# Kernel tuning notes

Hardware: AMD Instinct MI355X
Metric: run time of the kernel (lower is better)

Reference implementation:

```python
import jax, jax.numpy as jnp
import numpy as np

N = 50000
D_IN = 512
D_OUT = 512
NUM_SAMPLE = 2


def setup_inputs() -> dict:
    key = jax.random.key(0)
    ks = jax.random.split(key, 8)
    x = jax.random.normal(ks[0], (N, D_IN), dtype=jnp.float32)
    neighs1 = jax.random.randint(ks[1], (N, NUM_SAMPLE), 0, N, dtype=jnp.int32)
    neighs2 = jax.random.randint(ks[2], (N, NUM_SAMPLE), 0, N, dtype=jnp.int32)
    # SageLayer weights: [out, 2*in] (self || aggregated neighbors), xavier-ish scale
    W1 = jax.random.normal(ks[3], (D_OUT, 2 * D_IN), dtype=jnp.float32) * 0.03
    W2 = jax.random.normal(ks[4], (D_OUT, 2 * D_OUT), dtype=jnp.float32) * 0.03
    fc_w = jax.random.normal(ks[5], (2, N * D_OUT), dtype=jnp.float32) * 0.0005
    fc_b = jnp.zeros((2,), dtype=jnp.float32)
    return {"x": x, "neighs1": neighs1, "neighs2": neighs2,
            "W1": W1, "W2": W2, "fc_w": fc_w, "fc_b": fc_b}


def _sage_layer(h, neighs, W):
    # MEAN aggregation over the num_sample sampled neighbors (self excluded, gcn=False).
    # Equivalent to the original dense one-hot mask.div(num_neigh).mm(embed_matrix).
    agg = h[neighs].mean(axis=1)                      # [N, S, d] -> [N, d]
    combined = jnp.concatenate([h, agg], axis=1)      # [N, 2d]
    # F.relu(W.mm(combined.t())).t() == relu(combined @ W.T)
    return jax.nn.relu(combined @ W.T)                # [N, out]


def reference(x, neighs1, neighs2, W1, W2, fc_w, fc_b):
    h = _sage_layer(x, neighs1, W1)
    h = _sage_layer(h, neighs2, W2)
    flat = h.reshape(1, -1)                           # [1, N*out]
    logits = flat @ fc_w.T + fc_b                     # [1, 2]
    return (flat, jax.nn.log_softmax(logits, axis=1))
```

## Files before the change

### kernel.cpp

```cpp
#include <hip/hip_runtime.h>
#include <stdint.h>

typedef short bf16x8 __attribute__((ext_vector_type(8)));
typedef float f32x4 __attribute__((ext_vector_type(4)));
typedef unsigned short u16x8 __attribute__((ext_vector_type(8)));

#define N_NODES 50000
#define DIM 512
#define KDIM 1024
#define NPAD 50048
#define M_TILES 391
#define N_TILES 4
#define FLAT_TOTAL 25600000ULL

__device__ __forceinline__ unsigned short f2bf(float f) {
    unsigned u = __float_as_uint(f);
    unsigned r = u + 0x7FFFu + ((u >> 16) & 1u);
    return (unsigned short)(r >> 16);
}
__device__ __forceinline__ float bf2f(unsigned short h) {
    return __uint_as_float(((unsigned)h) << 16);
}

__device__ __forceinline__ void llds16(const void* g, void* l) {
    __builtin_amdgcn_global_load_lds(
        (const __attribute__((address_space(1))) void*)g,
        (__attribute__((address_space(3))) void*)l,
        16, 0, 0);
}

__global__ void cast_w(const float* __restrict__ w, unsigned short* __restrict__ o) {
    int i = (blockIdx.x * blockDim.x + threadIdx.x) * 8;
    float4 v0 = *(const float4*)&w[i];
    float4 v1 = *(const float4*)&w[i + 4];
    u16x8 r;
    r[0] = f2bf(v0.x); r[1] = f2bf(v0.y); r[2] = f2bf(v0.z); r[3] = f2bf(v0.w);
    r[4] = f2bf(v1.x); r[5] = f2bf(v1.y); r[6] = f2bf(v1.z); r[7] = f2bf(v1.w);
    *(u16x8*)&o[i] = r;
}

__global__ void build_a1(const float* __restrict__ x, const int* __restrict__ nb,
                         unsigned short* __restrict__ A) {
    int i = blockIdx.x;
    int t = threadIdx.x;
    u16x8 o;
    if (t < 64) {
        int c = t * 8;
        const float4* p = (const float4*)&x[(size_t)i * DIM + c];
        float4 a = p[0], b = p[1];
        o[0] = f2bf(a.x); o[1] = f2bf(a.y); o[2] = f2bf(a.z); o[3] = f2bf(a.w);
        o[4] = f2bf(b.x); o[5] = f2bf(b.y); o[6] = f2bf(b.z); o[7] = f2bf(b.w);
        *(u16x8*)&A[(size_t)i * KDIM + c] = o;
    } else {
        int c = (t - 64) * 8;
        int n0 = nb[i * 2], n1 = nb[i * 2 + 1];
        const float4* p0 = (const float4*)&x[(size_t)n0 * DIM + c];
        const float4* p1 = (const float4*)&x[(size_t)n1 * DIM + c];
        float4 a0 = p0[0], a1 = p0[1], b0 = p1[0], b1 = p1[1];
        o[0] = f2bf((a0.x + b0.x) * 0.5f); o[1] = f2bf((a0.y + b0.y) * 0.5f);
        o[2] = f2bf((a0.z + b0.z) * 0.5f); o[3] = f2bf((a0.w + b0.w) * 0.5f);
        o[4] = f2bf((a1.x + b1.x) * 0.5f); o[5] = f2bf((a1.y + b1.y) * 0.5f);
        o[6] = f2bf((a1.z + b1.z) * 0.5f); o[7] = f2bf((a1.w + b1.w) * 0.5f);
        *(u16x8*)&A[(size_t)i * KDIM + DIM + c] = o;
    }
}

__global__ void build_a2(const unsigned short* __restrict__ h, const int* __restrict__ nb,
                         unsigned short* __restrict__ A) {
    int i = blockIdx.x;
    int t = threadIdx.x;
    if (t < 64) {
        int c = t * 8;
        *(u16x8*)&A[(size_t)i * KDIM + c] = *(const u16x8*)&h[(size_t)i * DIM + c];
    } else {
        int c = (t - 64) * 8;
        int n0 = nb[i * 2], n1 = nb[i * 2 + 1];
        u16x8 a = *(const u16x8*)&h[(size_t)n0 * DIM + c];
        u16x8 b = *(const u16x8*)&h[(size_t)n1 * DIM + c];
        u16x8 o;
#pragma unroll
        for (int j = 0; j < 8; j++) o[j] = f2bf((bf2f(a[j]) + bf2f(b[j])) * 0.5f);
        *(u16x8*)&A[(size_t)i * KDIM + DIM + c] = o;
    }
}

template <int OUT_MODE>
__global__ __launch_bounds__(256)
void gemm_bt(const unsigned short* __restrict__ A, const unsigned short* __restrict__ B,
             void* __restrict__ C) {
    __shared__ unsigned short As[128 * 32];
    __shared__ unsigned short Bs[128 * 32];

    int t = threadIdx.x;
    int bm = blockIdx.x >> 2;
    int bn = blockIdx.x & 3;
    int lane = t & 63;
    int wave = t >> 6;
    int m_off = (wave >> 1) * 64;
    int n_off = (wave & 1) * 64;
    int lrow = lane & 15;
    int lk = (lane >> 4) * 8;

    f32x4 acc[4][4];
#pragma unroll
    for (int i = 0; i < 4; i++)
#pragma unroll
        for (int j = 0; j < 4; j++) acc[i][j] = (f32x4){0.f, 0.f, 0.f, 0.f};

    const unsigned short* ga = A + (size_t)(bm * 128 + (t >> 2)) * KDIM + (t & 3) * 8;
    const unsigned short* gb = B + (size_t)(bn * 128 + (t >> 2)) * KDIM + (t & 3) * 8;

    for (int k0 = 0; k0 < KDIM; k0 += 32) {
        __syncthreads();
        llds16(ga + k0, &As[t * 8]);
        llds16(ga + k0 + 64 * KDIM, &As[t * 8 + 2048]);
        llds16(gb + k0, &Bs[t * 8]);
        llds16(gb + k0 + 64 * KDIM, &Bs[t * 8 + 2048]);
        __syncthreads();

        bf16x8 af[4], bfr[4];
#pragma unroll
        for (int i = 0; i < 4; i++)
            af[i] = *(const bf16x8*)&As[(m_off + i * 16 + lrow) * 32 + lk];
#pragma unroll
        for (int j = 0; j < 4; j++)
            bfr[j] = *(const bf16x8*)&Bs[(n_off + j * 16 + lrow) * 32 + lk];
#pragma unroll
        for (int i = 0; i < 4; i++)
#pragma unroll
            for (int j = 0; j < 4; j++)
                acc[i][j] = __builtin_amdgcn_mfma_f32_16x16x32_bf16(af[i], bfr[j], acc[i][j], 0, 0, 0);
    }

    int lc = lane & 15;
    int lr = (lane >> 4) << 2;
#pragma unroll
    for (int i = 0; i < 4; i++) {
        int row0 = bm * 128 + m_off + i * 16 + lr;
#pragma unroll
        for (int j = 0; j < 4; j++) {
            int col = bn * 128 + n_off + j * 16 + lc;
            f32x4 v = acc[i][j];
            if (OUT_MODE == 0) {
                unsigned short* Cb = (unsigned short*)C;
#pragma unroll
                for (int r = 0; r < 4; r++)
                    Cb[(size_t)(row0 + r) * DIM + col] = f2bf(fmaxf(v[r], 0.f));
            } else {
                float* Cf = (float*)C;
#pragma unroll
                for (int r = 0; r < 4; r++)
                    if (row0 + r < N_NODES)
                        Cf[(size_t)(row0 + r) * DIM + col] = fmaxf(v[r], 0.f);
            }
        }
    }
}

__global__ void zero2(float* p) { if (threadIdx.x < 2) p[threadIdx.x] = 0.f; }

__global__ void fc_reduce(const float* __restrict__ flat, const float* __restrict__ fcw,
                          float* __restrict__ partials) {
    float s0 = 0.f, s1 = 0.f;
    size_t stride = (size_t)gridDim.x * blockDim.x * 4;
    for (size_t i = ((size_t)blockIdx.x * blockDim.x + threadIdx.x) * 4; i < FLAT_TOTAL; i += stride) {
        float4 v  = *(const float4*)&flat[i];
        float4 w0 = *(const float4*)&fcw[i];
        float4 w1 = *(const float4*)&fcw[FLAT_TOTAL + i];
        s0 += v.x * w0.x + v.y * w0.y + v.z * w0.z + v.w * w0.w;
        s1 += v.x * w1.x + v.y * w1.y + v.z * w1.z + v.w * w1.w;
    }
#pragma unroll
    for (int off = 32; off > 0; off >>= 1) {
        s0 += __shfl_down(s0, off);
        s1 += __shfl_down(s1, off);
    }
    __shared__ float r0[4], r1[4];
    int lane = threadIdx.x & 63, w = threadIdx.x >> 6;
    if (lane == 0) { r0[w] = s0; r1[w] = s1; }
    __syncthreads();
    if (threadIdx.x == 0) {
        atomicAdd(&partials[0], r0[0] + r0[1] + r0[2] + r0[3]);
        atomicAdd(&partials[1], r1[0] + r1[1] + r1[2] + r1[3]);
    }
}

__global__ void finalize(const float* __restrict__ partials, const float* __restrict__ fcb,
                         float* __restrict__ out2) {
    float l0 = partials[0] + fcb[0];
    float l1 = partials[1] + fcb[1];
    float m = fmaxf(l0, l1);
    float lse = m + logf(expf(l0 - m) + expf(l1 - m));
    out2[0] = l0 - lse;
    out2[1] = l1 - lse;
}

extern "C" void kernel_launch(void* const* d_in, const int* in_sizes, int n_in,
                              void* d_out, int out_size, void* d_ws, size_t ws_size,
                              hipStream_t stream) {
    const float* x   = (const float*)d_in[0];
    const int*   n1  = (const int*)d_in[1];
    const int*   n2  = (const int*)d_in[2];
    const float* W1  = (const float*)d_in[3];
    const float* W2  = (const float*)d_in[4];
    const float* fcw = (const float*)d_in[5];
    const float* fcb = (const float*)d_in[6];
    float* out = (float*)d_out;

    char* ws = (char*)d_ws;
    const size_t A_OFF   = 0;
    const size_t H1_OFF  = A_OFF + (size_t)NPAD * KDIM * 2;
    const size_t W1_OFF  = H1_OFF + (size_t)NPAD * DIM * 2;
    const size_t W2_OFF  = W1_OFF + (size_t)DIM * KDIM * 2;
    const size_t P_OFF   = W2_OFF + (size_t)DIM * KDIM * 2;
    unsigned short* Abuf = (unsigned short*)(ws + A_OFF);
    unsigned short* H1   = (unsigned short*)(ws + H1_OFF);
    unsigned short* W1b  = (unsigned short*)(ws + W1_OFF);
    unsigned short* W2b  = (unsigned short*)(ws + W2_OFF);
    float* partials      = (float*)(ws + P_OFF);

    zero2<<<1, 64, 0, stream>>>(partials);
    cast_w<<<256, 256, 0, stream>>>(W1, W1b);
    cast_w<<<256, 256, 0, stream>>>(W2, W2b);

    build_a1<<<N_NODES, 128, 0, stream>>>(x, n1, Abuf);
    gemm_bt<0><<<M_TILES * N_TILES, 256, 0, stream>>>(Abuf, W1b, H1);
    build_a2<<<N_NODES, 128, 0, stream>>>(H1, n2, Abuf);
    gemm_bt<1><<<M_TILES * N_TILES, 256, 0, stream>>>(Abuf, W2b, out);

    fc_reduce<<<2048, 256, 0, stream>>>(out, fcw, partials);
    finalize<<<1, 1, 0, stream>>>(partials, fcb, out + FLAT_TOTAL);
}
```

Before: 636.5 us.

## Apply weights before neighbor aggregation and fuse FC reduction into combine

Each layer is rewritten from relu([h, mean(h[nb])] @ W^T) into one GEMM h @ [W_self; W_neigh]^T that produces a 1024-wide intermediate T, followed by a gather-combine kernel that adds the self half to the mean of the neighbor halves and applies ReLU. This removes the build_a gather kernels that wrote a 1024-wide concatenated input; the GEMM now has K=512 and an N twice as wide, so the FLOPs stay the same. The second combine writes the fp32 output and also computes the FC dot products, storing per-block partials that a single-block kernel reduces. This avoids rereading the 100MB output and drops the atomics. The cost is that the intermediate T is written and gathered in bf16, which adds rounding before the ReLU.

```diff
diff --git a/kernel.cpp b/kernel.cpp
--- a/kernel.cpp
+++ b/kernel.cpp
@@ -7,11 +7,12 @@
 
 #define N_NODES 50000
 #define DIM 512
-#define KDIM 1024
+#define TDIM 1024
 #define NPAD 50048
 #define M_TILES 391
-#define N_TILES 4
+#define N_TILES 8
 #define FLAT_TOTAL 25600000ULL
+#define NBLK_COMB 12500
 
 __device__ __forceinline__ unsigned short f2bf(float f) {
     unsigned u = __float_as_uint(f);
@@ -29,71 +30,38 @@
         16, 0, 0);
 }
 
-__global__ void cast_w(const float* __restrict__ w, unsigned short* __restrict__ o) {
-    int i = (blockIdx.x * blockDim.x + threadIdx.x) * 8;
-    float4 v0 = *(const float4*)&w[i];
-    float4 v1 = *(const float4*)&w[i + 4];
+__global__ void cast_x(const float* __restrict__ x, unsigned short* __restrict__ o) {
+    size_t i = ((size_t)blockIdx.x * blockDim.x + threadIdx.x) * 8;
+    float4 v0 = *(const float4*)&x[i];
+    float4 v1 = *(const float4*)&x[i + 4];
     u16x8 r;
     r[0] = f2bf(v0.x); r[1] = f2bf(v0.y); r[2] = f2bf(v0.z); r[3] = f2bf(v0.w);
     r[4] = f2bf(v1.x); r[5] = f2bf(v1.y); r[6] = f2bf(v1.z); r[7] = f2bf(v1.w);
     *(u16x8*)&o[i] = r;
 }
 
-__global__ void build_a1(const float* __restrict__ x, const int* __restrict__ nb,
-                         unsigned short* __restrict__ A) {
-    int i = blockIdx.x;
-    int t = threadIdx.x;
-    u16x8 o;
-    if (t < 64) {
-        int c = t * 8;
-        const float4* p = (const float4*)&x[(size_t)i * DIM + c];
-        float4 a = p[0], b = p[1];
-        o[0] = f2bf(a.x); o[1] = f2bf(a.y); o[2] = f2bf(a.z); o[3] = f2bf(a.w);
-        o[4] = f2bf(b.x); o[5] = f2bf(b.y); o[6] = f2bf(b.z); o[7] = f2bf(b.w);
-        *(u16x8*)&A[(size_t)i * KDIM + c] = o;
-    } else {
-        int c = (t - 64) * 8;
-        int n0 = nb[i * 2], n1 = nb[i * 2 + 1];
-        const float4* p0 = (const float4*)&x[(size_t)n0 * DIM + c];
-        const float4* p1 = (const float4*)&x[(size_t)n1 * DIM + c];
-        float4 a0 = p0[0], a1 = p0[1], b0 = p1[0], b1 = p1[1];
-        o[0] = f2bf((a0.x + b0.x) * 0.5f); o[1] = f2bf((a0.y + b0.y) * 0.5f);
-        o[2] = f2bf((a0.z + b0.z) * 0.5f); o[3] = f2bf((a0.w + b0.w) * 0.5f);
-        o[4] = f2bf((a1.x + b1.x) * 0.5f); o[5] = f2bf((a1.y + b1.y) * 0.5f);
-        o[6] = f2bf((a1.z + b1.z) * 0.5f); o[7] = f2bf((a1.w + b1.w) * 0.5f);
-        *(u16x8*)&A[(size_t)i * KDIM + DIM + c] = o;
-    }
-}
-
-__global__ void build_a2(const unsigned short* __restrict__ h, const int* __restrict__ nb,
-                         unsigned short* __restrict__ A) {
-    int i = blockIdx.x;
-    int t = threadIdx.x;
-    if (t < 64) {
-        int c = t * 8;
-        *(u16x8*)&A[(size_t)i * KDIM + c] = *(const u16x8*)&h[(size_t)i * DIM + c];
-    } else {
-        int c = (t - 64) * 8;
-        int n0 = nb[i * 2], n1 = nb[i * 2 + 1];
-        u16x8 a = *(const u16x8*)&h[(size_t)n0 * DIM + c];
-        u16x8 b = *(const u16x8*)&h[(size_t)n1 * DIM + c];
-        u16x8 o;
-#pragma unroll
-        for (int j = 0; j < 8; j++) o[j] = f2bf((bf2f(a[j]) + bf2f(b[j])) * 0.5f);
-        *(u16x8*)&A[(size_t)i * KDIM + DIM + c] = o;
-    }
-}
-
-template <int OUT_MODE>
+__global__ void cast_w_split(const float* __restrict__ w, unsigned short* __restrict__ o) {
+    int idx = (blockIdx.x * 256 + threadIdx.x) * 8;
+    int j = idx >> 9;
+    int k = idx & 511;
+    size_t src = (j < 512) ? ((size_t)j * 1024 + k) : ((size_t)(j - 512) * 1024 + 512 + k);
+    float4 v0 = *(const float4*)&w[src];
+    float4 v1 = *(const float4*)&w[src + 4];
+    u16x8 r;
+    r[0] = f2bf(v0.x); r[1] = f2bf(v0.y); r[2] = f2bf(v0.z); r[3] = f2bf(v0.w);
+    r[4] = f2bf(v1.x); r[5] = f2bf(v1.y); r[6] = f2bf(v1.z); r[7] = f2bf(v1.w);
+    *(u16x8*)&o[idx] = r;
+}
+
 __global__ __launch_bounds__(256)
-void gemm_bt(const unsigned short* __restrict__ A, const unsigned short* __restrict__ B,
-             void* __restrict__ C) {
+void gemm_nt(const unsigned short* __restrict__ A, const unsigned short* __restrict__ B,
+             unsigned short* __restrict__ T) {
     __shared__ unsigned short As[128 * 32];
     __shared__ unsigned short Bs[128 * 32];
 
     int t = threadIdx.x;
-    int bm = blockIdx.x >> 2;
-    int bn = blockIdx.x & 3;
+    int bm = blockIdx.x >> 3;
+    int bn = blockIdx.x & 7;
     int lane = t & 63;
     int wave = t >> 6;
     int m_off = (wave >> 1) * 64;
@@ -107,15 +75,15 @@
 #pragma unroll
         for (int j = 0; j < 4; j++) acc[i][j] = (f32x4){0.f, 0.f, 0.f, 0.f};
 
-    const unsigned short* ga = A + (size_t)(bm * 128 + (t >> 2)) * KDIM + (t & 3) * 8;
-    const unsigned short* gb = B + (size_t)(bn * 128 + (t >> 2)) * KDIM + (t & 3) * 8;
-
-    for (int k0 = 0; k0 < KDIM; k0 += 32) {
+    const unsigned short* ga = A + (size_t)(bm * 128 + (t >> 2)) * DIM + (t & 3) * 8;
+    const unsigned short* gb = B + (size_t)(bn * 128 + (t >> 2)) * DIM + (t & 3) * 8;
+
+    for (int k0 = 0; k0 < DIM; k0 += 32) {
         __syncthreads();
         llds16(ga + k0, &As[t * 8]);
-        llds16(ga + k0 + 64 * KDIM, &As[t * 8 + 2048]);
+        llds16(ga + k0 + 64 * DIM, &As[t * 8 + 2048]);
         llds16(gb + k0, &Bs[t * 8]);
-        llds16(gb + k0 + 64 * KDIM, &Bs[t * 8 + 2048]);
+        llds16(gb + k0 + 64 * DIM, &Bs[t * 8 + 2048]);
         __syncthreads();
 
         bf16x8 af[4], bfr[4];
@@ -141,58 +109,95 @@
         for (int j = 0; j < 4; j++) {
             int col = bn * 128 + n_off + j * 16 + lc;
             f32x4 v = acc[i][j];
-            if (OUT_MODE == 0) {
-                unsigned short* Cb = (unsigned short*)C;
-#pragma unroll
-                for (int r = 0; r < 4; r++)
-                    Cb[(size_t)(row0 + r) * DIM + col] = f2bf(fmaxf(v[r], 0.f));
-            } else {
-                float* Cf = (float*)C;
-#pragma unroll
-                for (int r = 0; r < 4; r++)
-                    if (row0 + r < N_NODES)
-                        Cf[(size_t)(row0 + r) * DIM + col] = fmaxf(v[r], 0.f);
-            }
+#pragma unroll
+            for (int r = 0; r < 4; r++)
+                T[(size_t)(row0 + r) * TDIM + col] = f2bf(v[r]);
         }
     }
 }
 
-__global__ void zero2(float* p) { if (threadIdx.x < 2) p[threadIdx.x] = 0.f; }
-
-__global__ void fc_reduce(const float* __restrict__ flat, const float* __restrict__ fcw,
-                          float* __restrict__ partials) {
-    float s0 = 0.f, s1 = 0.f;
-    size_t stride = (size_t)gridDim.x * blockDim.x * 4;
-    for (size_t i = ((size_t)blockIdx.x * blockDim.x + threadIdx.x) * 4; i < FLAT_TOTAL; i += stride) {
-        float4 v  = *(const float4*)&flat[i];
-        float4 w0 = *(const float4*)&fcw[i];
-        float4 w1 = *(const float4*)&fcw[FLAT_TOTAL + i];
-        s0 += v.x * w0.x + v.y * w0.y + v.z * w0.z + v.w * w0.w;
-        s1 += v.x * w1.x + v.y * w1.y + v.z * w1.z + v.w * w1.w;
-    }
+__global__ void combine1(const unsigned short* __restrict__ T, const int* __restrict__ nb,
+                         unsigned short* __restrict__ H) {
+    int t = threadIdx.x;
+    int i = blockIdx.x * 4 + (t >> 6);
+    int lane = t & 63;
+    int c = lane * 8;
+    int n0 = nb[i * 2], n1 = nb[i * 2 + 1];
+    u16x8 p  = *(const u16x8*)&T[(size_t)i  * TDIM + c];
+    u16x8 q0 = *(const u16x8*)&T[(size_t)n0 * TDIM + 512 + c];
+    u16x8 q1 = *(const u16x8*)&T[(size_t)n1 * TDIM + 512 + c];
+    u16x8 o;
+#pragma unroll
+    for (int j = 0; j < 8; j++)
+        o[j] = f2bf(fmaxf(bf2f(p[j]) + 0.5f * (bf2f(q0[j]) + bf2f(q1[j])), 0.f));
+    *(u16x8*)&H[(size_t)i * DIM + c] = o;
+}
+
+__global__ void combine2(const unsigned short* __restrict__ T, const int* __restrict__ nb,
+                         const float* __restrict__ fcw, float* __restrict__ out,
+                         float2* __restrict__ partials) {
+    int t = threadIdx.x;
+    int i = blockIdx.x * 4 + (t >> 6);
+    int lane = t & 63;
+    int w = t >> 6;
+    int c = lane * 8;
+    int n0 = nb[i * 2], n1 = nb[i * 2 + 1];
+    u16x8 p  = *(const u16x8*)&T[(size_t)i  * TDIM + c];
+    u16x8 q0 = *(const u16x8*)&T[(size_t)n0 * TDIM + 512 + c];
+    u16x8 q1 = *(const u16x8*)&T[(size_t)n1 * TDIM + 512 + c];
+    float v[8];
+#pragma unroll
+    for (int j = 0; j < 8; j++)
+        v[j] = fmaxf(bf2f(p[j]) + 0.5f * (bf2f(q0[j]) + bf2f(q1[j])), 0.f);
+    size_t ob = (size_t)i * DIM + c;
+    *(float4*)&out[ob]     = (float4){v[0], v[1], v[2], v[3]};
+    *(float4*)&out[ob + 4] = (float4){v[4], v[5], v[6], v[7]};
+    float4 a0 = *(const float4*)&fcw[ob];
+    float4 a1 = *(const float4*)&fcw[ob + 4];
+    float4 b0 = *(const float4*)&fcw[FLAT_TOTAL + ob];
+    float4 b1 = *(const float4*)&fcw[FLAT_TOTAL + ob + 4];
+    float s0 = v[0]*a0.x + v[1]*a0.y + v[2]*a0.z + v[3]*a0.w
+             + v[4]*a1.x + v[5]*a1.y + v[6]*a1.z + v[7]*a1.w;
+    float s1 = v[0]*b0.x + v[1]*b0.y + v[2]*b0.z + v[3]*b0.w
+             + v[4]*b1.x + v[5]*b1.y + v[6]*b1.z + v[7]*b1.w;
 #pragma unroll
     for (int off = 32; off > 0; off >>= 1) {
         s0 += __shfl_down(s0, off);
         s1 += __shfl_down(s1, off);
     }
     __shared__ float r0[4], r1[4];
+    if (lane == 0) { r0[w] = s0; r1[w] = s1; }
+    __syncthreads();
+    if (t == 0)
+        partials[blockIdx.x] = make_float2(r0[0] + r0[1] + r0[2] + r0[3],
+                                           r1[0] + r1[1] + r1[2] + r1[3]);
+}
+
+__global__ void reduce_finalize(const float2* __restrict__ partials, const float* __restrict__ fcb,
+                                float* __restrict__ out2) {
+    float s0 = 0.f, s1 = 0.f;
+    for (int k = threadIdx.x; k < NBLK_COMB; k += 1024) {
+        float2 pr = partials[k];
+        s0 += pr.x; s1 += pr.y;
+    }
+#pragma unroll
+    for (int off = 32; off > 0; off >>= 1) {
+        s0 += __shfl_down(s0, off);
+        s1 += __shfl_down(s1, off);
+    }
+    __shared__ float r0[16], r1[16];
     int lane = threadIdx.x & 63, w = threadIdx.x >> 6;
     if (lane == 0) { r0[w] = s0; r1[w] = s1; }
     __syncthreads();
     if (threadIdx.x == 0) {
-        atomicAdd(&partials[0], r0[0] + r0[1] + r0[2] + r0[3]);
-        atomicAdd(&partials[1], r1[0] + r1[1] + r1[2] + r1[3]);
-    }
-}
-
-__global__ void finalize(const float* __restrict__ partials, const float* __restrict__ fcb,
-                         float* __restrict__ out2) {
-    float l0 = partials[0] + fcb[0];
-    float l1 = partials[1] + fcb[1];
-    float m = fmaxf(l0, l1);
-    float lse = m + logf(expf(l0 - m) + expf(l1 - m));
-    out2[0] = l0 - lse;
-    out2[1] = l1 - lse;
+        float l0 = fcb[0], l1 = fcb[1];
+#pragma unroll
+        for (int k = 0; k < 16; k++) { l0 += r0[k]; l1 += r1[k]; }
+        float m = fmaxf(l0, l1);
+        float lse = m + logf(expf(l0 - m) + expf(l1 - m));
+        out2[0] = l0 - lse;
+        out2[1] = l1 - lse;
+    }
 }
 
 extern "C" void kernel_launch(void* const* d_in, const int* in_sizes, int n_in,
@@ -208,26 +213,27 @@
     float* out = (float*)d_out;
 
     char* ws = (char*)d_ws;
-    const size_t A_OFF   = 0;
-    const size_t H1_OFF  = A_OFF + (size_t)NPAD * KDIM * 2;
+    const size_t XB_OFF  = 0;
+    const size_t T_OFF   = XB_OFF + (size_t)NPAD * DIM * 2;
+    const size_t H1_OFF  = T_OFF + (size_t)NPAD * TDIM * 2;
     const size_t W1_OFF  = H1_OFF + (size_t)NPAD * DIM * 2;
-    const size_t W2_OFF  = W1_OFF + (size_t)DIM * KDIM * 2;
-    const size_t P_OFF   = W2_OFF + (size_t)DIM * KDIM * 2;
-    unsigned short* Abuf = (unsigned short*)(ws + A_OFF);
-    unsigned short* H1   = (unsigned short*)(ws + H1_OFF);
-    unsigned short* W1b  = (unsigned short*)(ws + W1_OFF);
-    unsigned short* W2b  = (unsigned short*)(ws + W2_OFF);
-    float* partials      = (float*)(ws + P_OFF);
-
-    zero2<<<1, 64, 0, stream>>>(partials);
-    cast_w<<<256, 256, 0, stream>>>(W1, W1b);
-    cast_w<<<256, 256, 0, stream>>>(W2, W2b);
-
-    build_a1<<<N_NODES, 128, 0, stream>>>(x, n1, Abuf);
-    gemm_bt<0><<<M_TILES * N_TILES, 256, 0, stream>>>(Abuf, W1b, H1);
-    build_a2<<<N_NODES, 128, 0, stream>>>(H1, n2, Abuf);
-    gemm_bt<1><<<M_TILES * N_TILES, 256, 0, stream>>>(Abuf, W2b, out);
-
-    fc_reduce<<<2048, 256, 0, stream>>>(out, fcw, partials);
-    finalize<<<1, 1, 0, stream>>>(partials, fcb, out + FLAT_TOTAL);
-}
+    const size_t W2_OFF  = W1_OFF + (size_t)TDIM * DIM * 2;
+    const size_t P_OFF   = W2_OFF + (size_t)TDIM * DIM * 2;
+    unsigned short* Xb  = (unsigned short*)(ws + XB_OFF);
+    unsigned short* T   = (unsigned short*)(ws + T_OFF);
+    unsigned short* H1  = (unsigned short*)(ws + H1_OFF);
+    unsigned short* W1s = (unsigned short*)(ws + W1_OFF);
+    unsigned short* W2s = (unsigned short*)(ws + W2_OFF);
+    float2* partials    = (float2*)(ws + P_OFF);
+
+    cast_w_split<<<256, 256, 0, stream>>>(W1, W1s);
+    cast_w_split<<<256, 256, 0, stream>>>(W2, W2s);
+    cast_x<<<12500, 256, 0, stream>>>(x, Xb);
+
+    gemm_nt<<<M_TILES * N_TILES, 256, 0, stream>>>(Xb, W1s, T);
+    combine1<<<NBLK_COMB, 256, 0, stream>>>(T, n1, H1);
+    gemm_nt<<<M_TILES * N_TILES, 256, 0, stream>>>(H1, W2s, T);
+    combine2<<<NBLK_COMB, 256, 0, stream>>>(T, n2, fcw, out, partials);
+
+    reduce_finalize<<<1, 1024, 0, stream>>>(partials, fcb, out + FLAT_TOTAL);
+}
```

Result: faster. 585.6 us (-8.0%).
